# Kernel optimization log

Measured on AMD Instinct MI355X. Metric: run time of the kernel, lower is better.

Reference implementation:

```python
import jax, jax.numpy as jnp
import numpy as np

B, S, H = 2, 1024, 1024
NH, NKV, HD = 16, 4, 64
E, K, I = 8, 2, 3584
EPS = 1e-5
THETA = 1e6


def setup_inputs() -> dict:
    key = jax.random.key(0)
    ks = jax.random.split(key, 12)
    sc = 0.02
    return {
        "hidden_states": jax.random.normal(ks[0], (B, S, H), jnp.float32),
        "ln1_w": jnp.ones((H,), jnp.float32),
        "wq": jax.random.normal(ks[1], (H, NH * HD), jnp.float32) * sc,
        "wk": jax.random.normal(ks[2], (H, NKV * HD), jnp.float32) * sc,
        "wv": jax.random.normal(ks[3], (H, NKV * HD), jnp.float32) * sc,
        "wo": jax.random.normal(ks[4], (NH * HD, H), jnp.float32) * sc,
        "ln2_w": jnp.ones((H,), jnp.float32),
        "router_w": jax.random.normal(ks[5], (H, E), jnp.float32) * sc,
        "w_gate": jax.random.normal(ks[6], (E, H, I), jnp.float32) * sc,
        "w_up": jax.random.normal(ks[7], (E, H, I), jnp.float32) * sc,
        "w_down": jax.random.normal(ks[8], (E, I, H), jnp.float32) * sc,
    }


def _rmsnorm(x, w):
    xf = x.astype(jnp.float32)
    return (xf * jax.lax.rsqrt(jnp.mean(xf * xf, axis=-1, keepdims=True) + EPS)).astype(x.dtype) * w


def _rope_cos_sin():
    inv_freq = 1.0 / (THETA ** (jnp.arange(0, HD, 2, dtype=jnp.float32) / HD))
    ang = jnp.arange(S, dtype=jnp.float32)[:, None] * inv_freq[None, :]  # [S, HD//2]
    emb = jnp.concatenate([ang, ang], axis=-1)  # [S, HD]
    return jnp.cos(emb)[None, :, None, :], jnp.sin(emb)[None, :, None, :]


def _rotate_half(x):
    return jnp.concatenate([-x[..., HD // 2:], x[..., : HD // 2]], axis=-1)


def _attention(x, wq, wk, wv, wo):
    q = (x @ wq).reshape(B, S, NH, HD)
    k = (x @ wk).reshape(B, S, NKV, HD)
    v = (x @ wv).reshape(B, S, NKV, HD)
    cos, sin = _rope_cos_sin()
    q = q * cos + _rotate_half(q) * sin
    k = k * cos + _rotate_half(k) * sin
    rep = NH // NKV
    k = jnp.repeat(k, rep, axis=2)  # [B,S,NH,HD]
    v = jnp.repeat(v, rep, axis=2)
    scores = jnp.einsum("bqhd,bkhd->bhqk", q, k) / jnp.sqrt(jnp.float32(HD))
    causal = jnp.tril(jnp.ones((S, S), bool))
    scores = jnp.where(causal[None, None], scores, jnp.float32(-1e9))
    probs = jax.nn.softmax(scores, axis=-1)
    out = jnp.einsum("bhqk,bkhd->bqhd", probs, v).reshape(B, S, NH * HD)
    return out @ wo


def _moe(x, router_w, w_gate, w_up, w_down):
    t = x.reshape(B * S, H)  # [T,H]
    logits = t @ router_w  # [T,E]
    probs = jax.nn.softmax(logits.astype(jnp.float32), axis=-1)
    top_v, top_i = jax.lax.top_k(probs, K)
    top_v = top_v / jnp.sum(top_v, axis=-1, keepdims=True)  # normalize_top_k_affinities
    # dense combine weights [T,E]
    dense_w = jnp.sum(jax.nn.one_hot(top_i, E, dtype=t.dtype) * top_v[..., None], axis=1)
    out = jnp.zeros_like(t)
    for e in range(E):  # small fixed expert loop (E=8)
        g = jax.nn.silu(t @ w_gate[e]) * (t @ w_up[e])
        out = out + dense_w[:, e:e + 1] * (g @ w_down[e])
    return out.reshape(B, S, H)


def reference(hidden_states, ln1_w, wq, wk, wv, wo, ln2_w, router_w, w_gate, w_up, w_down):
    residual = hidden_states
    h = _rmsnorm(hidden_states, ln1_w)
    h = residual + _attention(h, wq, wk, wv, wo)
    residual = h
    h2 = _rmsnorm(h, ln2_w)
    h = residual + _moe(h2, router_w, w_gate, w_up, w_down)
    return h
```

## Files before the change

kernel.cpp:

```cpp
#include <hip/hip_runtime.h>
#include <hip/hip_bf16.h>
#include <math.h>

#define B_ 2
#define S_ 1024
#define H_ 1024
#define NH_ 16
#define NKV_ 4
#define HD_ 64
#define E_ 8
#define I_ 3584
#define T_ (B_*S_)

#define BM 64
#define BN 64
#define BK 32
#define MBM 128
#define DBM 64
#define MBK 64

typedef __bf16 bf16x8 __attribute__((ext_vector_type(8)));
typedef float f32x4 __attribute__((ext_vector_type(4)));

__device__ __forceinline__ __bf16 bf_hi(float f) { return (__bf16)f; }
__device__ __forceinline__ __bf16 bf_lo(float f, __bf16 h) { return (__bf16)(f - (float)h); }

__device__ __forceinline__ int swz(int row, int col) {
    return (row * 64 + col * 2) ^ (((row >> 3) & 7) << 4);
}
__device__ __forceinline__ int swz128(int row, int col) {
    return (row * 128 + col * 2) ^ ((row & 7) << 4);
}

__global__ __launch_bounds__(256) void cvt_bf16_kernel(
    const float* __restrict__ src, __bf16* __restrict__ dst, int n8)
{
    int idx = blockIdx.x * 256 + threadIdx.x;
    if (idx >= n8) return;
    const float4* s = (const float4*)src + (size_t)idx * 2;
    float4 a = s[0], b = s[1];
    bf16x8 v;
    v[0] = (__bf16)a.x; v[1] = (__bf16)a.y; v[2] = (__bf16)a.z; v[3] = (__bf16)a.w;
    v[4] = (__bf16)b.x; v[5] = (__bf16)b.y; v[6] = (__bf16)b.z; v[7] = (__bf16)b.w;
    ((bf16x8*)dst)[idx] = v;
}

__global__ __launch_bounds__(256) void transpose_cvt_kernel(
    const float* __restrict__ src, __bf16* __restrict__ dst, int M, int N)
{
    int e = blockIdx.z;
    src += (size_t)e * M * N;
    dst += (size_t)e * M * N;
    int n0 = blockIdx.x * 64, m0 = blockIdx.y * 64;
    __shared__ __bf16 Ts[64][72];
    int tid = threadIdx.x;
#pragma unroll
    for (int i = 0; i < 16; i++) {
        int row = i * 4 + (tid >> 6);
        int col = tid & 63;
        Ts[row][col] = (__bf16)src[(size_t)(m0 + row) * N + n0 + col];
    }
    __syncthreads();
#pragma unroll
    for (int j = 0; j < 2; j++) {
        int n = (tid >> 3) + j * 32;
        int k8 = (tid & 7) * 8;
        bf16x8 v;
#pragma unroll
        for (int ii = 0; ii < 8; ii++) v[ii] = Ts[k8 + ii][n];
        *(bf16x8*)(dst + (size_t)(n0 + n) * M + m0 + k8) = v;
    }
}

__global__ __launch_bounds__(256) void rmsnorm_kernel(
    const float* __restrict__ x, const float* __restrict__ w, float* __restrict__ out)
{
    int row = blockIdx.x;
    int tid = threadIdx.x;
    const float* xr = x + (size_t)row * H_;
    float vals[4];
    float ss = 0.f;
#pragma unroll
    for (int i = 0; i < 4; i++) {
        vals[i] = xr[tid + 256 * i];
        ss += vals[i] * vals[i];
    }
#pragma unroll
    for (int off = 32; off; off >>= 1) ss += __shfl_xor(ss, off);
    __shared__ float red[4];
    int wid = tid >> 6;
    if ((tid & 63) == 0) red[wid] = ss;
    __syncthreads();
    float tot = red[0] + red[1] + red[2] + red[3];
    float scale = rsqrtf(tot * (1.0f / H_) + 1e-5f);
#pragma unroll
    for (int i = 0; i < 4; i++)
        out[(size_t)row * H_ + tid + 256 * i] = vals[i] * scale * w[tid + 256 * i];
}

__global__ __launch_bounds__(256) void gemm_bf16(
    const float* __restrict__ A, const float* __restrict__ Bm,
    float* __restrict__ C, const float* __restrict__ res,
    int M, int N, int Kd)
{
    __shared__ __bf16 As[BM * BK];
    __shared__ __bf16 Bs[BN * BK];
    char* Asb = (char*)As;
    char* Bsb = (char*)Bs;
    int tid = threadIdx.x;
    int lane = tid & 63, wid = tid >> 6;
    int wm = wid >> 1, wn = wid & 1;
    int m0 = blockIdx.y * BM, n0 = blockIdx.x * BN;
    f32x4 acc[2][2] = {};
    int ar = tid >> 2, ac = (tid & 3) * 8;
    int bk = tid >> 3, bc = (tid & 7) * 8;
    for (int kt = 0; kt < Kd; kt += BK) {
        const float* ag = A + (size_t)(m0 + ar) * Kd + kt + ac;
        bf16x8 av;
#pragma unroll
        for (int i = 0; i < 8; i++) av[i] = (__bf16)ag[i];
        *(bf16x8*)(Asb + swz(ar, ac)) = av;
        const float* bg = Bm + (size_t)(kt + bk) * N + n0 + bc;
#pragma unroll
        for (int i = 0; i < 8; i++)
            *(__bf16*)(Bsb + swz(bc + i, bk)) = (__bf16)bg[i];
        __syncthreads();
        int r = lane & 15, k8 = (lane >> 4) * 8;
        bf16x8 af[2], bfr[2];
#pragma unroll
        for (int m = 0; m < 2; m++) af[m] = *(const bf16x8*)(Asb + swz(wm * 32 + m * 16 + r, k8));
#pragma unroll
        for (int n = 0; n < 2; n++) bfr[n] = *(const bf16x8*)(Bsb + swz(wn * 32 + n * 16 + r, k8));
#pragma unroll
        for (int m = 0; m < 2; m++)
#pragma unroll
            for (int n = 0; n < 2; n++)
                acc[m][n] = __builtin_amdgcn_mfma_f32_16x16x32_bf16(af[m], bfr[n], acc[m][n], 0, 0, 0);
        __syncthreads();
    }
    int cl = lane & 15, rb = (lane >> 4) * 4;
#pragma unroll
    for (int m = 0; m < 2; m++)
#pragma unroll
        for (int n = 0; n < 2; n++)
#pragma unroll
            for (int j = 0; j < 4; j++) {
                int row = m0 + wm * 32 + m * 16 + rb + j;
                int col = n0 + wn * 32 + n * 16 + cl;
                size_t o = (size_t)row * N + col;
                float v = acc[m][n][j];
                if (res) v += res[o];
                C[o] = v;
            }
}

__global__ void rope_kernel(float* __restrict__ x, int heads, int total)
{
    int idx = blockIdx.x * blockDim.x + threadIdx.x;
    if (idx >= total) return;
    int j = idx & 31;
    int th = idx >> 5;
    int h = th % heads;
    int t = th / heads;
    int s = t & (S_ - 1);
    float inv = powf(1e6f, -(float)j / 32.0f);
    float ang = (float)s * inv;
    float c = cosf(ang), sn = sinf(ang);
    size_t base = (size_t)t * heads * HD_ + (size_t)h * HD_;
    float x1 = x[base + j], x2 = x[base + 32 + j];
    x[base + j] = x1 * c - x2 * sn;
    x[base + 32 + j] = x2 * c + x1 * sn;
}

#define LP 72
__global__ __launch_bounds__(256) void flash_kernel(
    const float* __restrict__ q, const float* __restrict__ k,
    const float* __restrict__ v, float* __restrict__ o)
{
    __shared__ __bf16 Ks [64][LP];
    __shared__ __bf16 Ksl[64][LP];
    __shared__ __bf16 Vt [64][LP];
    __shared__ __bf16 Vtl[64][LP];
    __shared__ __bf16 Pl [4][16][LP];
    __shared__ __bf16 Pll[4][16][LP];

    int tid = threadIdx.x;
    int lane = tid & 63, wid = tid >> 6;
    int qr = lane & 15, quad = lane >> 4;
    int qt = (S_ / 16 - 1) - blockIdx.x;
    int kvh = blockIdx.y, b = blockIdx.z;
    int h = kvh * 4 + wid;
    int s0 = qt * 16;

    const float* qg = q + ((size_t)(b * S_ + s0 + qr) * NH_ + h) * HD_ + quad * 8;
    bf16x8 qf[2], qlo[2];
#pragma unroll
    for (int ks = 0; ks < 2; ks++)
#pragma unroll
        for (int i = 0; i < 8; i++) {
            float f = qg[ks * 32 + i] * 0.125f;
            __bf16 hh = bf_hi(f);
            qf[ks][i] = hh;
            qlo[ks][i] = bf_lo(f, hh);
        }

    float m_run[4], l_run[4];
    f32x4 o_acc[4] = {};
#pragma unroll
    for (int j = 0; j < 4; j++) { m_run[j] = -1e30f; l_run[j] = 0.f; }

    int skey = tid >> 2, shd0 = (tid & 3) * 16;
    int vhd = tid & 63, vkey0 = (tid >> 6) * 16;

    for (int kt = 0; kt <= s0 + 15; kt += 64) {
        __syncthreads();
        {
            const float* kg = k + ((size_t)(b * S_ + kt + skey) * NKV_ + kvh) * HD_ + shd0;
#pragma unroll
            for (int i = 0; i < 16; i++) {
                float f = kg[i];
                __bf16 hh = bf_hi(f);
                Ks [skey][shd0 + i] = hh;
                Ksl[skey][shd0 + i] = bf_lo(f, hh);
            }
        }
        {
            const float* vg = v + ((size_t)(b * S_ + kt + vkey0) * NKV_ + kvh) * HD_ + vhd;
#pragma unroll
            for (int i = 0; i < 16; i++) {
                float val = vg[(size_t)i * (NKV_ * HD_)];
                __bf16 hh = bf_hi(val);
                Vt [vhd][vkey0 + i] = hh;
                Vtl[vhd][vkey0 + i] = bf_lo(val, hh);
            }
        }
        __syncthreads();

        f32x4 sc4[4];
#pragma unroll
        for (int sub = 0; sub < 4; sub++) {
            int krow = sub * 16 + qr;
            bf16x8 kh0 = *(const bf16x8*)&Ks [krow][quad * 8];
            bf16x8 kh1 = *(const bf16x8*)&Ks [krow][32 + quad * 8];
            bf16x8 kl0 = *(const bf16x8*)&Ksl[krow][quad * 8];
            bf16x8 kl1 = *(const bf16x8*)&Ksl[krow][32 + quad * 8];
            f32x4 z = {};
            z = __builtin_amdgcn_mfma_f32_16x16x32_bf16(qf[0],  kh0, z, 0, 0, 0);
            z = __builtin_amdgcn_mfma_f32_16x16x32_bf16(qf[1],  kh1, z, 0, 0, 0);
            z = __builtin_amdgcn_mfma_f32_16x16x32_bf16(qlo[0], kh0, z, 0, 0, 0);
            z = __builtin_amdgcn_mfma_f32_16x16x32_bf16(qlo[1], kh1, z, 0, 0, 0);
            z = __builtin_amdgcn_mfma_f32_16x16x32_bf16(qf[0],  kl0, z, 0, 0, 0);
            z = __builtin_amdgcn_mfma_f32_16x16x32_bf16(qf[1],  kl1, z, 0, 0, 0);
            sc4[sub] = z;
        }
        if (kt + 63 > s0) {
#pragma unroll
            for (int sub = 0; sub < 4; sub++)
#pragma unroll
                for (int j = 0; j < 4; j++) {
                    int key = kt + sub * 16 + qr;
                    int row = s0 + quad * 4 + j;
                    if (key > row) sc4[sub][j] = -1e30f;
                }
        }
#pragma unroll
        for (int j = 0; j < 4; j++) {
            float mx = fmaxf(fmaxf(sc4[0][j], sc4[1][j]), fmaxf(sc4[2][j], sc4[3][j]));
#pragma unroll
            for (int off = 1; off < 16; off <<= 1) mx = fmaxf(mx, __shfl_xor(mx, off));
            float mn = fmaxf(m_run[j], mx);
            float scale = __expf(m_run[j] - mn);
            m_run[j] = mn;
            float rs = 0.f;
#pragma unroll
            for (int sub = 0; sub < 4; sub++) {
                float pe = __expf(sc4[sub][j] - mn);
                sc4[sub][j] = pe;
                rs += pe;
            }
#pragma unroll
            for (int off = 1; off < 16; off <<= 1) rs += __shfl_xor(rs, off);
            l_run[j] = l_run[j] * scale + rs;
#pragma unroll
            for (int sub = 0; sub < 4; sub++) o_acc[sub][j] *= scale;
        }
#pragma unroll
        for (int sub = 0; sub < 4; sub++)
#pragma unroll
            for (int j = 0; j < 4; j++) {
                float pe = sc4[sub][j];
                __bf16 hh = bf_hi(pe);
                Pl [wid][quad * 4 + j][sub * 16 + qr] = hh;
                Pll[wid][quad * 4 + j][sub * 16 + qr] = bf_lo(pe, hh);
            }
        __syncthreads();
        bf16x8 ph0 = *(const bf16x8*)&Pl [wid][qr][quad * 8];
        bf16x8 ph1 = *(const bf16x8*)&Pl [wid][qr][32 + quad * 8];
        bf16x8 pl0 = *(const bf16x8*)&Pll[wid][qr][quad * 8];
        bf16x8 pl1 = *(const bf16x8*)&Pll[wid][qr][32 + quad * 8];
#pragma unroll
        for (int sub = 0; sub < 4; sub++) {
            int vrow = sub * 16 + qr;
            bf16x8 vh0 = *(const bf16x8*)&Vt [vrow][quad * 8];
            bf16x8 vh1 = *(const bf16x8*)&Vt [vrow][32 + quad * 8];
            bf16x8 vl0 = *(const bf16x8*)&Vtl[vrow][quad * 8];
            bf16x8 vl1 = *(const bf16x8*)&Vtl[vrow][32 + quad * 8];
            o_acc[sub] = __builtin_amdgcn_mfma_f32_16x16x32_bf16(ph0, vh0, o_acc[sub], 0, 0, 0);
            o_acc[sub] = __builtin_amdgcn_mfma_f32_16x16x32_bf16(ph1, vh1, o_acc[sub], 0, 0, 0);
            o_acc[sub] = __builtin_amdgcn_mfma_f32_16x16x32_bf16(ph0, vl0, o_acc[sub], 0, 0, 0);
            o_acc[sub] = __builtin_amdgcn_mfma_f32_16x16x32_bf16(ph1, vl1, o_acc[sub], 0, 0, 0);
            o_acc[sub] = __builtin_amdgcn_mfma_f32_16x16x32_bf16(pl0, vh0, o_acc[sub], 0, 0, 0);
            o_acc[sub] = __builtin_amdgcn_mfma_f32_16x16x32_bf16(pl1, vh1, o_acc[sub], 0, 0, 0);
        }
    }
#pragma unroll
    for (int j = 0; j < 4; j++) {
        float inv = 1.f / l_run[j];
        int row = s0 + quad * 4 + j;
#pragma unroll
        for (int sub = 0; sub < 4; sub++)
            o[((size_t)(b * S_ + row) * NH_ + h) * HD_ + sub * 16 + qr] = o_acc[sub][j] * inv;
    }
}

__global__ __launch_bounds__(256) void router_kernel(
    const float* __restrict__ xn, const float* __restrict__ rw,
    int* __restrict__ top_i, float* __restrict__ top_w)
{
    int wid = threadIdx.x >> 6, lane = threadIdx.x & 63;
    int t = blockIdx.x * 4 + wid;
    const float* xr = xn + (size_t)t * H_;
    float acc[E_] = {};
    for (int c = 0; c < H_ / 64; c++) {
        float xd = xr[c * 64 + lane];
        const float* wrow = rw + (size_t)(c * 64 + lane) * E_;
#pragma unroll
        for (int e = 0; e < E_; e++) acc[e] += xd * wrow[e];
    }
#pragma unroll
    for (int e = 0; e < E_; e++) {
        float r = acc[e];
#pragma unroll
        for (int off = 32; off; off >>= 1) r += __shfl_xor(r, off);
        acc[e] = r;
    }
    if (lane == 0) {
        float mx = acc[0];
        for (int e = 1; e < E_; e++) mx = fmaxf(mx, acc[e]);
        float p[E_], sum = 0.f;
        for (int e = 0; e < E_; e++) { p[e] = __expf(acc[e] - mx); sum += p[e]; }
        float inv_s = 1.f / sum;
        for (int e = 0; e < E_; e++) p[e] *= inv_s;
        int i0 = 0;
        for (int e = 1; e < E_; e++) if (p[e] > p[i0]) i0 = e;
        int i1 = (i0 == 0) ? 1 : 0;
        for (int e = 0; e < E_; e++) if (e != i0 && p[e] > p[i1]) i1 = e;
        float v0 = p[i0], v1 = p[i1], inv = 1.f / (v0 + v1);
        top_i[t * 2] = i0; top_i[t * 2 + 1] = i1;
        top_w[t * 2] = v0 * inv; top_w[t * 2 + 1] = v1 * inv;
    }
}

__global__ void assign_kernel(
    const int* __restrict__ top_i, const float* __restrict__ top_w,
    int* __restrict__ tlist, int* __restrict__ pair_pos,
    int* __restrict__ counts, int* __restrict__ offsets)
{
    __shared__ int cnt[E_], off[E_], fill[E_];
    int tid = threadIdx.x;
    if (tid < E_) { cnt[tid] = 0; fill[tid] = 0; }
    __syncthreads();
    for (int t = tid; t < T_; t += 256) {
        atomicAdd(&cnt[top_i[t * 2]], 1);
        atomicAdd(&cnt[top_i[t * 2 + 1]], 1);
    }
    __syncthreads();
    if (tid == 0) {
        int o = 0;
        for (int e = 0; e < E_; e++) { off[e] = o; o += cnt[e]; }
    }
    __syncthreads();
    for (int t = tid; t < T_; t += 256) {
        for (int j = 0; j < 2; j++) {
            int e = top_i[t * 2 + j];
            int pos = off[e] + atomicAdd(&fill[e], 1);
            tlist[pos] = t;
            pair_pos[t * 2 + j] = pos;
        }
    }
    __syncthreads();
    if (tid < E_) { counts[tid] = cnt[tid]; offsets[tid] = off[tid]; }
}

__global__ __launch_bounds__(256) void moe_gemm_gateup(
    const __bf16* __restrict__ Xb, const __bf16* __restrict__ WgT, const __bf16* __restrict__ WuT,
    __bf16* __restrict__ act, const int* __restrict__ tlist,
    const int* __restrict__ counts, const int* __restrict__ offsets)
{
    int e = blockIdx.z;
    int cnt = counts[e], off = offsets[e];
    int m0 = blockIdx.y * MBM;
    if (m0 >= cnt) return;
    int n0 = blockIdx.x * BN;
    const __bf16* Bg = WgT + (size_t)e * H_ * I_;
    const __bf16* Bu = WuT + (size_t)e * H_ * I_;
    __shared__ __bf16 As[MBM * MBK];
    __shared__ __bf16 Gs[BN * MBK];
    __shared__ __bf16 Us[BN * MBK];
    __shared__ int rowidx[MBM];
    char* Asb = (char*)As;
    char* Gsb = (char*)Gs;
    char* Usb = (char*)Us;
    int tid = threadIdx.x;
    if (tid < MBM) {
        int rl = m0 + tid;
        rowidx[tid] = tlist[off + ((rl < cnt) ? rl : 0)];
    }
    __syncthreads();
    int lane = tid & 63, wid = tid >> 6;
    f32x4 accg[2][4] = {}, accu[2][4] = {};
    int ar = tid >> 1, ac = (tid & 1) * 32;
    int bn = tid >> 2, bc = (tid & 3) * 16;
    const __bf16* abase = Xb + (size_t)rowidx[ar] * H_ + ac;
    const __bf16* gbase = Bg + (size_t)(n0 + bn) * H_ + bc;
    const __bf16* ubase = Bu + (size_t)(n0 + bn) * H_ + bc;
    bf16x8 pa[4], pg[2], pu[2];
#pragma unroll
    for (int g = 0; g < 4; g++) pa[g] = *(const bf16x8*)(abase + g * 8);
#pragma unroll
    for (int g = 0; g < 2; g++) {
        pg[g] = *(const bf16x8*)(gbase + g * 8);
        pu[g] = *(const bf16x8*)(ubase + g * 8);
    }
    for (int kt = 0; kt < H_; kt += MBK) {
#pragma unroll
        for (int g = 0; g < 4; g++) *(bf16x8*)(Asb + swz128(ar, ac + g * 8)) = pa[g];
#pragma unroll
        for (int g = 0; g < 2; g++) {
            *(bf16x8*)(Gsb + swz128(bn, bc + g * 8)) = pg[g];
            *(bf16x8*)(Usb + swz128(bn, bc + g * 8)) = pu[g];
        }
        __syncthreads();
        int kn = kt + MBK;
        if (kn < H_) {
#pragma unroll
            for (int g = 0; g < 4; g++) pa[g] = *(const bf16x8*)(abase + kn + g * 8);
#pragma unroll
            for (int g = 0; g < 2; g++) {
                pg[g] = *(const bf16x8*)(gbase + kn + g * 8);
                pu[g] = *(const bf16x8*)(ubase + kn + g * 8);
            }
        }
        int r = lane & 15, q8 = (lane >> 4) * 8;
#pragma unroll
        for (int kk = 0; kk < 2; kk++) {
            bf16x8 af[2], gf[4], uf[4];
#pragma unroll
            for (int m = 0; m < 2; m++)
                af[m] = *(const bf16x8*)(Asb + swz128(wid * 32 + m * 16 + r, kk * 32 + q8));
#pragma unroll
            for (int n = 0; n < 4; n++) {
                gf[n] = *(const bf16x8*)(Gsb + swz128(n * 16 + r, kk * 32 + q8));
                uf[n] = *(const bf16x8*)(Usb + swz128(n * 16 + r, kk * 32 + q8));
            }
#pragma unroll
            for (int m = 0; m < 2; m++)
#pragma unroll
                for (int n = 0; n < 4; n++) {
                    accg[m][n] = __builtin_amdgcn_mfma_f32_16x16x32_bf16(af[m], gf[n], accg[m][n], 0, 0, 0);
                    accu[m][n] = __builtin_amdgcn_mfma_f32_16x16x32_bf16(af[m], uf[n], accu[m][n], 0, 0, 0);
                }
        }
        __syncthreads();
    }
    int cl = lane & 15, rb = (lane >> 4) * 4;
#pragma unroll
    for (int m = 0; m < 2; m++)
#pragma unroll
        for (int n = 0; n < 4; n++)
#pragma unroll
            for (int j = 0; j < 4; j++) {
                int rl = m0 + wid * 32 + m * 16 + rb + j;
                if (rl >= cnt) continue;
                int col = n0 + n * 16 + cl;
                float g = accg[m][n][j], u = accu[m][n][j];
                float sig = 1.f / (1.f + __expf(-g));
                act[(size_t)(off + rl) * I_ + col] = (__bf16)(g * sig * u);
            }
}

__global__ __launch_bounds__(256) void moe_gemm_down(
    const __bf16* __restrict__ act, const __bf16* __restrict__ WdT,
    float* __restrict__ dout, const int* __restrict__ counts, const int* __restrict__ offsets)
{
    int e = blockIdx.z;
    int cnt = counts[e], off = offsets[e];
    int m0 = blockIdx.y * DBM;
    if (m0 >= cnt) return;
    int n0 = blockIdx.x * BN;
    const __bf16* Bw = WdT + (size_t)e * I_ * H_;
    __shared__ __bf16 As[DBM * MBK];
    __shared__ __bf16 Bs[BN * MBK];
    char* Asb = (char*)As;
    char* Bsb = (char*)Bs;
    int tid = threadIdx.x;
    int lane = tid & 63, wid = tid >> 6;
    f32x4 acc[4] = {};
    int ar = tid >> 2, ac = (tid & 3) * 16;
    int bn = tid >> 2, bc = (tid & 3) * 16;
    int arow = m0 + ar; if (arow >= cnt) arow = cnt - 1;
    const __bf16* abase = act + (size_t)(off + arow) * I_ + ac;
    const __bf16* bbase = Bw + (size_t)(n0 + bn) * I_ + bc;
    bf16x8 pa[2], pb[2];
#pragma unroll
    for (int g = 0; g < 2; g++) {
        pa[g] = *(const bf16x8*)(abase + g * 8);
        pb[g] = *(const bf16x8*)(bbase + g * 8);
    }
    for (int kt = 0; kt < I_; kt += MBK) {
#pragma unroll
        for (int g = 0; g < 2; g++) {
            *(bf16x8*)(Asb + swz128(ar, ac + g * 8)) = pa[g];
            *(bf16x8*)(Bsb + swz128(bn, bc + g * 8)) = pb[g];
        }
        __syncthreads();
        int kn = kt + MBK;
        if (kn < I_) {
#pragma unroll
            for (int g = 0; g < 2; g++) {
                pa[g] = *(const bf16x8*)(abase + kn + g * 8);
                pb[g] = *(const bf16x8*)(bbase + kn + g * 8);
            }
        }
        int r = lane & 15, q8 = (lane >> 4) * 8;
#pragma unroll
        for (int kk = 0; kk < 2; kk++) {
            bf16x8 af = *(const bf16x8*)(Asb + swz128(wid * 16 + r, kk * 32 + q8));
            bf16x8 bfr[4];
#pragma unroll
            for (int n = 0; n < 4; n++)
                bfr[n] = *(const bf16x8*)(Bsb + swz128(n * 16 + r, kk * 32 + q8));
#pragma unroll
            for (int n = 0; n < 4; n++)
                acc[n] = __builtin_amdgcn_mfma_f32_16x16x32_bf16(af, bfr[n], acc[n], 0, 0, 0);
        }
        __syncthreads();
    }
    int cl = lane & 15, rb = (lane >> 4) * 4;
#pragma unroll
    for (int n = 0; n < 4; n++)
#pragma unroll
        for (int j = 0; j < 4; j++) {
            int rl = m0 + wid * 16 + rb + j;
            if (rl >= cnt) continue;
            int col = n0 + n * 16 + cl;
            dout[(size_t)(off + rl) * H_ + col] = acc[n][j];
        }
}

__global__ __launch_bounds__(256) void combine_kernel(
    const float* __restrict__ hres, const float* __restrict__ dout,
    const int* __restrict__ pair_pos, const float* __restrict__ top_w,
    float* __restrict__ out)
{
    int idx = blockIdx.x * 256 + threadIdx.x;
    int t = idx >> 10, d = idx & 1023;
    float v = hres[idx];
    int p0 = pair_pos[t * 2], p1 = pair_pos[t * 2 + 1];
    v += top_w[t * 2] * dout[(size_t)p0 * H_ + d]
       + top_w[t * 2 + 1] * dout[(size_t)p1 * H_ + d];
    out[idx] = v;
}

extern "C" void kernel_launch(void* const* d_in, const int* in_sizes, int n_in,
                              void* d_out, int out_size, void* d_ws, size_t ws_size,
                              hipStream_t stream) {
    const float* hidden = (const float*)d_in[0];
    const float* ln1 = (const float*)d_in[1];
    const float* wq = (const float*)d_in[2];
    const float* wk = (const float*)d_in[3];
    const float* wv = (const float*)d_in[4];
    const float* wo = (const float*)d_in[5];
    const float* ln2 = (const float*)d_in[6];
    const float* rw = (const float*)d_in[7];
    const float* wg = (const float*)d_in[8];
    const float* wu = (const float*)d_in[9];
    const float* wd = (const float*)d_in[10];
    float* out = (float*)d_out;

    char* ws = (char*)d_ws;
    size_t o = 0;
    auto alloc = [&](size_t bytes) -> void* {
        void* p = ws + o;
        o += (bytes + 255) & ~(size_t)255;
        return p;
    };
    float* xn   = (float*)alloc((size_t)T_ * H_ * 4);
    float* qb   = (float*)alloc((size_t)T_ * NH_ * HD_ * 4);
    float* kb   = (float*)alloc((size_t)T_ * NKV_ * HD_ * 4);
    float* vb   = (float*)alloc((size_t)T_ * NKV_ * HD_ * 4);
    float* attn = (float*)alloc((size_t)T_ * H_ * 4);
    float* hres = (float*)alloc((size_t)T_ * H_ * 4);
    int*   top_i    = (int*)alloc((size_t)T_ * 2 * 4);
    float* top_w    = (float*)alloc((size_t)T_ * 2 * 4);
    int*   pair_pos = (int*)alloc((size_t)T_ * 2 * 4);
    int*   tlist    = (int*)alloc((size_t)T_ * 2 * 4);
    int*   counts   = (int*)alloc(E_ * 4);
    int*   offsets  = (int*)alloc(E_ * 4);
    __bf16* actb  = (__bf16*)alloc((size_t)T_ * 2 * I_ * 2);
    float*  doutb = (float*)alloc((size_t)T_ * 2 * H_ * 4);
    __bf16* xnb = (__bf16*)alloc((size_t)T_ * H_ * 2);
    __bf16* wgt = (__bf16*)alloc((size_t)E_ * H_ * I_ * 2);
    __bf16* wut = (__bf16*)alloc((size_t)E_ * H_ * I_ * 2);
    __bf16* wdt = (__bf16*)alloc((size_t)E_ * I_ * H_ * 2);

    transpose_cvt_kernel<<<dim3(I_ / 64, H_ / 64, E_), 256, 0, stream>>>(wg, wgt, H_, I_);
    transpose_cvt_kernel<<<dim3(I_ / 64, H_ / 64, E_), 256, 0, stream>>>(wu, wut, H_, I_);
    transpose_cvt_kernel<<<dim3(H_ / 64, I_ / 64, E_), 256, 0, stream>>>(wd, wdt, I_, H_);

    rmsnorm_kernel<<<T_, 256, 0, stream>>>(hidden, ln1, xn);
    gemm_bf16<<<dim3((NH_ * HD_) / BN, T_ / BM), 256, 0, stream>>>(xn, wq, qb, nullptr, T_, NH_ * HD_, H_);
    gemm_bf16<<<dim3((NKV_ * HD_) / BN, T_ / BM), 256, 0, stream>>>(xn, wk, kb, nullptr, T_, NKV_ * HD_, H_);
    gemm_bf16<<<dim3((NKV_ * HD_) / BN, T_ / BM), 256, 0, stream>>>(xn, wv, vb, nullptr, T_, NKV_ * HD_, H_);
    {
        int tq = T_ * NH_ * 32, tk = T_ * NKV_ * 32;
        rope_kernel<<<(tq + 255) / 256, 256, 0, stream>>>(qb, NH_, tq);
        rope_kernel<<<(tk + 255) / 256, 256, 0, stream>>>(kb, NKV_, tk);
    }
    flash_kernel<<<dim3(S_ / 16, NKV_, B_), 256, 0, stream>>>(qb, kb, vb, attn);
    gemm_bf16<<<dim3(H_ / BN, T_ / BM), 256, 0, stream>>>(attn, wo, hres, hidden, T_, H_, H_);
    rmsnorm_kernel<<<T_, 256, 0, stream>>>(hres, ln2, xn);
    cvt_bf16_kernel<<<(T_ * H_ / 8 + 255) / 256, 256, 0, stream>>>(xn, xnb, T_ * H_ / 8);
    router_kernel<<<T_ / 4, 256, 0, stream>>>(xn, rw, top_i, top_w);
    assign_kernel<<<1, 256, 0, stream>>>(top_i, top_w, tlist, pair_pos, counts, offsets);
    moe_gemm_gateup<<<dim3(I_ / BN, T_ / MBM, E_), 256, 0, stream>>>(xnb, wgt, wut, actb, tlist, counts, offsets);
    moe_gemm_down<<<dim3(H_ / BN, T_ / DBM, E_), 256, 0, stream>>>(actb, wdt, doutb, counts, offsets);
    combine_kernel<<<(T_ * H_) / 256, 256, 0, stream>>>(hres, doutb, pair_pos, top_w, out);
}
```

Baseline: 500.0 us.

## Double-buffer shared memory in MoE gate/up and down GEMMs

Both MoE GEMM kernels now use two LDS buffers. The next K tile is written into the alternate buffer after the MFMA work on the current one, and the following tile is prefetched into registers. This removes one __syncthreads per K iteration and lets stores to shared memory overlap with compute. In exchange, LDS usage doubles, which can lower occupancy, and the loads are now issued after the MFMAs instead of before them, which may shorten the window for hiding latency.

```diff
diff --git a/kernel.cpp b/kernel.cpp
--- a/kernel.cpp
+++ b/kernel.cpp
@@ -404,13 +404,10 @@
     int n0 = blockIdx.x * BN;
     const __bf16* Bg = WgT + (size_t)e * H_ * I_;
     const __bf16* Bu = WuT + (size_t)e * H_ * I_;
-    __shared__ __bf16 As[MBM * MBK];
-    __shared__ __bf16 Gs[BN * MBK];
-    __shared__ __bf16 Us[BN * MBK];
+    __shared__ __bf16 As[2][MBM * MBK];
+    __shared__ __bf16 Gs[2][BN * MBK];
+    __shared__ __bf16 Us[2][BN * MBK];
     __shared__ int rowidx[MBM];
-    char* Asb = (char*)As;
-    char* Gsb = (char*)Gs;
-    char* Usb = (char*)Us;
     int tid = threadIdx.x;
     if (tid < MBM) {
         int rl = m0 + tid;
@@ -424,34 +421,36 @@
     const __bf16* abase = Xb + (size_t)rowidx[ar] * H_ + ac;
     const __bf16* gbase = Bg + (size_t)(n0 + bn) * H_ + bc;
     const __bf16* ubase = Bu + (size_t)(n0 + bn) * H_ + bc;
+    {
+        char* Asb = (char*)As[0];
+        char* Gsb = (char*)Gs[0];
+        char* Usb = (char*)Us[0];
+#pragma unroll
+        for (int g = 0; g < 4; g++)
+            *(bf16x8*)(Asb + swz128(ar, ac + g * 8)) = *(const bf16x8*)(abase + g * 8);
+#pragma unroll
+        for (int g = 0; g < 2; g++) {
+            *(bf16x8*)(Gsb + swz128(bn, bc + g * 8)) = *(const bf16x8*)(gbase + g * 8);
+            *(bf16x8*)(Usb + swz128(bn, bc + g * 8)) = *(const bf16x8*)(ubase + g * 8);
+        }
+    }
     bf16x8 pa[4], pg[2], pu[2];
-#pragma unroll
-    for (int g = 0; g < 4; g++) pa[g] = *(const bf16x8*)(abase + g * 8);
-#pragma unroll
-    for (int g = 0; g < 2; g++) {
-        pg[g] = *(const bf16x8*)(gbase + g * 8);
-        pu[g] = *(const bf16x8*)(ubase + g * 8);
-    }
+    if (H_ > MBK) {
+#pragma unroll
+        for (int g = 0; g < 4; g++) pa[g] = *(const bf16x8*)(abase + MBK + g * 8);
+#pragma unroll
+        for (int g = 0; g < 2; g++) {
+            pg[g] = *(const bf16x8*)(gbase + MBK + g * 8);
+            pu[g] = *(const bf16x8*)(ubase + MBK + g * 8);
+        }
+    }
+    int cur = 0;
+    int r = lane & 15, q8 = (lane >> 4) * 8;
     for (int kt = 0; kt < H_; kt += MBK) {
-#pragma unroll
-        for (int g = 0; g < 4; g++) *(bf16x8*)(Asb + swz128(ar, ac + g * 8)) = pa[g];
-#pragma unroll
-        for (int g = 0; g < 2; g++) {
-            *(bf16x8*)(Gsb + swz128(bn, bc + g * 8)) = pg[g];
-            *(bf16x8*)(Usb + swz128(bn, bc + g * 8)) = pu[g];
-        }
         __syncthreads();
-        int kn = kt + MBK;
-        if (kn < H_) {
-#pragma unroll
-            for (int g = 0; g < 4; g++) pa[g] = *(const bf16x8*)(abase + kn + g * 8);
-#pragma unroll
-            for (int g = 0; g < 2; g++) {
-                pg[g] = *(const bf16x8*)(gbase + kn + g * 8);
-                pu[g] = *(const bf16x8*)(ubase + kn + g * 8);
-            }
-        }
-        int r = lane & 15, q8 = (lane >> 4) * 8;
+        char* Asb = (char*)As[cur];
+        char* Gsb = (char*)Gs[cur];
+        char* Usb = (char*)Us[cur];
 #pragma unroll
         for (int kk = 0; kk < 2; kk++) {
             bf16x8 af[2], gf[4], uf[4];
@@ -471,7 +470,30 @@
                     accu[m][n] = __builtin_amdgcn_mfma_f32_16x16x32_bf16(af[m], uf[n], accu[m][n], 0, 0, 0);
                 }
         }
-        __syncthreads();
+        int kn = kt + MBK;
+        if (kn < H_) {
+            char* Asw = (char*)As[cur ^ 1];
+            char* Gsw = (char*)Gs[cur ^ 1];
+            char* Usw = (char*)Us[cur ^ 1];
+#pragma unroll
+            for (int g = 0; g < 4; g++) *(bf16x8*)(Asw + swz128(ar, ac + g * 8)) = pa[g];
+#pragma unroll
+            for (int g = 0; g < 2; g++) {
+                *(bf16x8*)(Gsw + swz128(bn, bc + g * 8)) = pg[g];
+                *(bf16x8*)(Usw + swz128(bn, bc + g * 8)) = pu[g];
+            }
+            int k2 = kn + MBK;
+            if (k2 < H_) {
+#pragma unroll
+                for (int g = 0; g < 4; g++) pa[g] = *(const bf16x8*)(abase + k2 + g * 8);
+#pragma unroll
+                for (int g = 0; g < 2; g++) {
+                    pg[g] = *(const bf16x8*)(gbase + k2 + g * 8);
+                    pu[g] = *(const bf16x8*)(ubase + k2 + g * 8);
+                }
+            }
+            cur ^= 1;
+        }
     }
     int cl = lane & 15, rb = (lane >> 4) * 4;
 #pragma unroll
@@ -499,10 +521,8 @@
     if (m0 >= cnt) return;
     int n0 = blockIdx.x * BN;
     const __bf16* Bw = WdT + (size_t)e * I_ * H_;
-    __shared__ __bf16 As[DBM * MBK];
-    __shared__ __bf16 Bs[BN * MBK];
-    char* Asb = (char*)As;
-    char* Bsb = (char*)Bs;
+    __shared__ __bf16 As[2][DBM * MBK];
+    __shared__ __bf16 Bs[2][BN * MBK];
     int tid = threadIdx.x;
     int lane = tid & 63, wid = tid >> 6;
     f32x4 acc[4] = {};
@@ -511,28 +531,29 @@
     int arow = m0 + ar; if (arow >= cnt) arow = cnt - 1;
     const __bf16* abase = act + (size_t)(off + arow) * I_ + ac;
     const __bf16* bbase = Bw + (size_t)(n0 + bn) * I_ + bc;
+    {
+        char* Asb = (char*)As[0];
+        char* Bsb = (char*)Bs[0];
+#pragma unroll
+        for (int g = 0; g < 2; g++) {
+            *(bf16x8*)(Asb + swz128(ar, ac + g * 8)) = *(const bf16x8*)(abase + g * 8);
+            *(bf16x8*)(Bsb + swz128(bn, bc + g * 8)) = *(const bf16x8*)(bbase + g * 8);
+        }
+    }
     bf16x8 pa[2], pb[2];
-#pragma unroll
-    for (int g = 0; g < 2; g++) {
-        pa[g] = *(const bf16x8*)(abase + g * 8);
-        pb[g] = *(const bf16x8*)(bbase + g * 8);
-    }
+    if (I_ > MBK) {
+#pragma unroll
+        for (int g = 0; g < 2; g++) {
+            pa[g] = *(const bf16x8*)(abase + MBK + g * 8);
+            pb[g] = *(const bf16x8*)(bbase + MBK + g * 8);
+        }
+    }
+    int cur = 0;
+    int r = lane & 15, q8 = (lane >> 4) * 8;
     for (int kt = 0; kt < I_; kt += MBK) {
-#pragma unroll
-        for (int g = 0; g < 2; g++) {
-            *(bf16x8*)(Asb + swz128(ar, ac + g * 8)) = pa[g];
-            *(bf16x8*)(Bsb + swz128(bn, bc + g * 8)) = pb[g];
-        }
         __syncthreads();
-        int kn = kt + MBK;
-        if (kn < I_) {
-#pragma unroll
-            for (int g = 0; g < 2; g++) {
-                pa[g] = *(const bf16x8*)(abase + kn + g * 8);
-                pb[g] = *(const bf16x8*)(bbase + kn + g * 8);
-            }
-        }
-        int r = lane & 15, q8 = (lane >> 4) * 8;
+        char* Asb = (char*)As[cur];
+        char* Bsb = (char*)Bs[cur];
 #pragma unroll
         for (int kk = 0; kk < 2; kk++) {
             bf16x8 af = *(const bf16x8*)(Asb + swz128(wid * 16 + r, kk * 32 + q8));
@@ -544,7 +565,25 @@
             for (int n = 0; n < 4; n++)
                 acc[n] = __builtin_amdgcn_mfma_f32_16x16x32_bf16(af, bfr[n], acc[n], 0, 0, 0);
         }
-        __syncthreads();
+        int kn = kt + MBK;
+        if (kn < I_) {
+            char* Asw = (char*)As[cur ^ 1];
+            char* Bsw = (char*)Bs[cur ^ 1];
+#pragma unroll
+            for (int g = 0; g < 2; g++) {
+                *(bf16x8*)(Asw + swz128(ar, ac + g * 8)) = pa[g];
+                *(bf16x8*)(Bsw + swz128(bn, bc + g * 8)) = pb[g];
+            }
+            int k2 = kn + MBK;
+            if (k2 < I_) {
+#pragma unroll
+                for (int g = 0; g < 2; g++) {
+                    pa[g] = *(const bf16x8*)(abase + k2 + g * 8);
+                    pb[g] = *(const bf16x8*)(bbase + k2 + g * 8);
+                }
+            }
+            cur ^= 1;
+        }
     }
     int cl = lane & 15, rb = (lane >> 4) * 4;
 #pragma unroll
```

Result: no change. 492.0 us (-1.6%).

## Enlarge MoE gate/up tile to 128x128 and double-buffer down-proj LDS

Applied to the files above, without the earlier changes.

The gate/up expert GEMM moves from a 128x64 to a 128x128 output tile, with a 2x2 warp layout where each warp computes 64x64 for both gate and up. This raises arithmetic intensity and halves redundant loads of the A tile, at the cost of twice the accumulator registers. The change adds launch_bounds(256,2), which may cause spills. The down-projection GEMM now double-buffers shared memory, so the next tile is written while the current one is computed, removing one barrier per k-step.

```diff
diff --git a/kernel.cpp b/kernel.cpp
--- a/kernel.cpp
+++ b/kernel.cpp
@@ -16,6 +16,7 @@
 #define BN 64
 #define BK 32
 #define MBM 128
+#define GBN 128
 #define DBM 64
 #define MBK 64
 
@@ -392,7 +393,7 @@
     if (tid < E_) { counts[tid] = cnt[tid]; offsets[tid] = off[tid]; }
 }
 
-__global__ __launch_bounds__(256) void moe_gemm_gateup(
+__global__ __launch_bounds__(256, 2) void moe_gemm_gateup(
     const __bf16* __restrict__ Xb, const __bf16* __restrict__ WgT, const __bf16* __restrict__ WuT,
     __bf16* __restrict__ act, const int* __restrict__ tlist,
     const int* __restrict__ counts, const int* __restrict__ offsets)
@@ -401,12 +402,12 @@
     int cnt = counts[e], off = offsets[e];
     int m0 = blockIdx.y * MBM;
     if (m0 >= cnt) return;
-    int n0 = blockIdx.x * BN;
+    int n0 = blockIdx.x * GBN;
     const __bf16* Bg = WgT + (size_t)e * H_ * I_;
     const __bf16* Bu = WuT + (size_t)e * H_ * I_;
     __shared__ __bf16 As[MBM * MBK];
-    __shared__ __bf16 Gs[BN * MBK];
-    __shared__ __bf16 Us[BN * MBK];
+    __shared__ __bf16 Gs[GBN * MBK];
+    __shared__ __bf16 Us[GBN * MBK];
     __shared__ int rowidx[MBM];
     char* Asb = (char*)As;
     char* Gsb = (char*)Gs;
@@ -418,25 +419,25 @@
     }
     __syncthreads();
     int lane = tid & 63, wid = tid >> 6;
-    f32x4 accg[2][4] = {}, accu[2][4] = {};
+    int wm = wid >> 1, wn = wid & 1;
+    f32x4 accg[4][4] = {}, accu[4][4] = {};
     int ar = tid >> 1, ac = (tid & 1) * 32;
-    int bn = tid >> 2, bc = (tid & 3) * 16;
+    int bn = tid >> 1, bc = (tid & 1) * 32;
     const __bf16* abase = Xb + (size_t)rowidx[ar] * H_ + ac;
     const __bf16* gbase = Bg + (size_t)(n0 + bn) * H_ + bc;
     const __bf16* ubase = Bu + (size_t)(n0 + bn) * H_ + bc;
-    bf16x8 pa[4], pg[2], pu[2];
-#pragma unroll
-    for (int g = 0; g < 4; g++) pa[g] = *(const bf16x8*)(abase + g * 8);
-#pragma unroll
-    for (int g = 0; g < 2; g++) {
+    bf16x8 pa[4], pg[4], pu[4];
+#pragma unroll
+    for (int g = 0; g < 4; g++) {
+        pa[g] = *(const bf16x8*)(abase + g * 8);
         pg[g] = *(const bf16x8*)(gbase + g * 8);
         pu[g] = *(const bf16x8*)(ubase + g * 8);
     }
+    int r = lane & 15, q8 = (lane >> 4) * 8;
     for (int kt = 0; kt < H_; kt += MBK) {
 #pragma unroll
-        for (int g = 0; g < 4; g++) *(bf16x8*)(Asb + swz128(ar, ac + g * 8)) = pa[g];
-#pragma unroll
-        for (int g = 0; g < 2; g++) {
+        for (int g = 0; g < 4; g++) {
+            *(bf16x8*)(Asb + swz128(ar, ac + g * 8)) = pa[g];
             *(bf16x8*)(Gsb + swz128(bn, bc + g * 8)) = pg[g];
             *(bf16x8*)(Usb + swz128(bn, bc + g * 8)) = pu[g];
         }
@@ -444,27 +445,25 @@
         int kn = kt + MBK;
         if (kn < H_) {
 #pragma unroll
-            for (int g = 0; g < 4; g++) pa[g] = *(const bf16x8*)(abase + kn + g * 8);
-#pragma unroll
-            for (int g = 0; g < 2; g++) {
+            for (int g = 0; g < 4; g++) {
+                pa[g] = *(const bf16x8*)(abase + kn + g * 8);
                 pg[g] = *(const bf16x8*)(gbase + kn + g * 8);
                 pu[g] = *(const bf16x8*)(ubase + kn + g * 8);
             }
         }
-        int r = lane & 15, q8 = (lane >> 4) * 8;
 #pragma unroll
         for (int kk = 0; kk < 2; kk++) {
-            bf16x8 af[2], gf[4], uf[4];
-#pragma unroll
-            for (int m = 0; m < 2; m++)
-                af[m] = *(const bf16x8*)(Asb + swz128(wid * 32 + m * 16 + r, kk * 32 + q8));
+            bf16x8 af[4], gf[4], uf[4];
+#pragma unroll
+            for (int m = 0; m < 4; m++)
+                af[m] = *(const bf16x8*)(Asb + swz128(wm * 64 + m * 16 + r, kk * 32 + q8));
 #pragma unroll
             for (int n = 0; n < 4; n++) {
-                gf[n] = *(const bf16x8*)(Gsb + swz128(n * 16 + r, kk * 32 + q8));
-                uf[n] = *(const bf16x8*)(Usb + swz128(n * 16 + r, kk * 32 + q8));
-            }
-#pragma unroll
-            for (int m = 0; m < 2; m++)
+                gf[n] = *(const bf16x8*)(Gsb + swz128(wn * 64 + n * 16 + r, kk * 32 + q8));
+                uf[n] = *(const bf16x8*)(Usb + swz128(wn * 64 + n * 16 + r, kk * 32 + q8));
+            }
+#pragma unroll
+            for (int m = 0; m < 4; m++)
 #pragma unroll
                 for (int n = 0; n < 4; n++) {
                     accg[m][n] = __builtin_amdgcn_mfma_f32_16x16x32_bf16(af[m], gf[n], accg[m][n], 0, 0, 0);
@@ -475,14 +474,14 @@
     }
     int cl = lane & 15, rb = (lane >> 4) * 4;
 #pragma unroll
-    for (int m = 0; m < 2; m++)
+    for (int m = 0; m < 4; m++)
 #pragma unroll
         for (int n = 0; n < 4; n++)
 #pragma unroll
             for (int j = 0; j < 4; j++) {
-                int rl = m0 + wid * 32 + m * 16 + rb + j;
+                int rl = m0 + wm * 64 + m * 16 + rb + j;
                 if (rl >= cnt) continue;
-                int col = n0 + n * 16 + cl;
+                int col = n0 + wn * 64 + n * 16 + cl;
                 float g = accg[m][n][j], u = accu[m][n][j];
                 float sig = 1.f / (1.f + __expf(-g));
                 act[(size_t)(off + rl) * I_ + col] = (__bf16)(g * sig * u);
@@ -499,10 +498,8 @@
     if (m0 >= cnt) return;
     int n0 = blockIdx.x * BN;
     const __bf16* Bw = WdT + (size_t)e * I_ * H_;
-    __shared__ __bf16 As[DBM * MBK];
-    __shared__ __bf16 Bs[BN * MBK];
-    char* Asb = (char*)As;
-    char* Bsb = (char*)Bs;
+    __shared__ __bf16 As[2][DBM * MBK];
+    __shared__ __bf16 Bs[2][BN * MBK];
     int tid = threadIdx.x;
     int lane = tid & 63, wid = tid >> 6;
     f32x4 acc[4] = {};
@@ -511,28 +508,29 @@
     int arow = m0 + ar; if (arow >= cnt) arow = cnt - 1;
     const __bf16* abase = act + (size_t)(off + arow) * I_ + ac;
     const __bf16* bbase = Bw + (size_t)(n0 + bn) * I_ + bc;
+    {
+        char* Asb = (char*)As[0];
+        char* Bsb = (char*)Bs[0];
+#pragma unroll
+        for (int g = 0; g < 2; g++) {
+            *(bf16x8*)(Asb + swz128(ar, ac + g * 8)) = *(const bf16x8*)(abase + g * 8);
+            *(bf16x8*)(Bsb + swz128(bn, bc + g * 8)) = *(const bf16x8*)(bbase + g * 8);
+        }
+    }
     bf16x8 pa[2], pb[2];
-#pragma unroll
-    for (int g = 0; g < 2; g++) {
-        pa[g] = *(const bf16x8*)(abase + g * 8);
-        pb[g] = *(const bf16x8*)(bbase + g * 8);
-    }
+    if (I_ > MBK) {
+#pragma unroll
+        for (int g = 0; g < 2; g++) {
+            pa[g] = *(const bf16x8*)(abase + MBK + g * 8);
+            pb[g] = *(const bf16x8*)(bbase + MBK + g * 8);
+        }
+    }
+    int cur = 0;
+    int r = lane & 15, q8 = (lane >> 4) * 8;
     for (int kt = 0; kt < I_; kt += MBK) {
-#pragma unroll
-        for (int g = 0; g < 2; g++) {
-            *(bf16x8*)(Asb + swz128(ar, ac + g * 8)) = pa[g];
-            *(bf16x8*)(Bsb + swz128(bn, bc + g * 8)) = pb[g];
-        }
-        __syncthreads();
-        int kn = kt + MBK;
-        if (kn < I_) {
-#pragma unroll
-            for (int g = 0; g < 2; g++) {
-                pa[g] = *(const bf16x8*)(abase + kn + g * 8);
-                pb[g] = *(const bf16x8*)(bbase + kn + g * 8);
-            }
-        }
-        int r = lane & 15, q8 = (lane >> 4) * 8;
+        __syncthreads();
+        char* Asb = (char*)As[cur];
+        char* Bsb = (char*)Bs[cur];
 #pragma unroll
         for (int kk = 0; kk < 2; kk++) {
             bf16x8 af = *(const bf16x8*)(Asb + swz128(wid * 16 + r, kk * 32 + q8));
@@ -544,7 +542,25 @@
             for (int n = 0; n < 4; n++)
                 acc[n] = __builtin_amdgcn_mfma_f32_16x16x32_bf16(af, bfr[n], acc[n], 0, 0, 0);
         }
-        __syncthreads();
+        int kn = kt + MBK;
+        if (kn < I_) {
+            char* Asw = (char*)As[cur ^ 1];
+            char* Bsw = (char*)Bs[cur ^ 1];
+#pragma unroll
+            for (int g = 0; g < 2; g++) {
+                *(bf16x8*)(Asw + swz128(ar, ac + g * 8)) = pa[g];
+                *(bf16x8*)(Bsw + swz128(bn, bc + g * 8)) = pb[g];
+            }
+            int k2 = kn + MBK;
+            if (k2 < I_) {
+#pragma unroll
+                for (int g = 0; g < 2; g++) {
+                    pa[g] = *(const bf16x8*)(abase + k2 + g * 8);
+                    pb[g] = *(const bf16x8*)(bbase + k2 + g * 8);
+                }
+            }
+            cur ^= 1;
+        }
     }
     int cl = lane & 15, rb = (lane >> 4) * 4;
 #pragma unroll
@@ -633,7 +649,7 @@
     cvt_bf16_kernel<<<(T_ * H_ / 8 + 255) / 256, 256, 0, stream>>>(xn, xnb, T_ * H_ / 8);
     router_kernel<<<T_ / 4, 256, 0, stream>>>(xn, rw, top_i, top_w);
     assign_kernel<<<1, 256, 0, stream>>>(top_i, top_w, tlist, pair_pos, counts, offsets);
-    moe_gemm_gateup<<<dim3(I_ / BN, T_ / MBM, E_), 256, 0, stream>>>(xnb, wgt, wut, actb, tlist, counts, offsets);
+    moe_gemm_gateup<<<dim3(I_ / GBN, T_ / MBM, E_), 256, 0, stream>>>(xnb, wgt, wut, actb, tlist, counts, offsets);
     moe_gemm_down<<<dim3(H_ / BN, T_ / DBM, E_), 256, 0, stream>>>(actb, wdt, doutb, counts, offsets);
     combine_kernel<<<(T_ * H_) / 256, 256, 0, stream>>>(hres, doutb, pair_pos, top_w, out);
 }
```

Result: slower. 521.5 us (+4.3%).
